# Optimization experiments

Hardware: AMD Instinct MI355X
Metric: run time of the kernel (lower is better)

Reference implementation:

```python
import jax, jax.numpy as jnp
import numpy as np

N_NODES = 100000
N_EDGES = 6400000


def setup_inputs() -> dict:
    key = jax.random.key(0)
    k1, k2, k3, k4, k5, k6 = jax.random.split(key, 6)
    edge_predictions = jax.random.normal(k1, (N_EDGES,), dtype=jnp.float32)
    node_predictions = jax.random.normal(k2, (N_NODES,), dtype=jnp.float32)
    x = jax.random.uniform(k3, (N_NODES, 4), dtype=jnp.float32)  # col 2 = demand
    capacity = jnp.ones((1,), dtype=jnp.float32) * 50.0  # vehicle capacity
    y_edges = (jax.random.uniform(k4, (N_EDGES,)) < 0.1).astype(jnp.float32)
    y_nodes = jax.random.normal(k5, (N_NODES,), dtype=jnp.float32)
    edge_index = jax.random.randint(k6, (2, N_EDGES), 0, N_NODES, dtype=jnp.int64)
    return {
        'edge_predictions': edge_predictions,
        'node_predictions': node_predictions,
        'x': x,
        'capacity': capacity,
        'y_edges': y_edges,
        'y_nodes': y_nodes,
        'edge_index': edge_index,
        'num_nodes': N_NODES,
    }


def _bce_with_logits(logits, targets):
    # numerically stable elementwise BCE-with-logits
    return jnp.maximum(logits, 0.0) - logits * targets + jnp.log1p(jnp.exp(-jnp.abs(logits)))


def _focal_loss(logits, targets, alpha=0.25, gamma=2.0):
    bce = _bce_with_logits(logits, targets)
    probs = jax.nn.sigmoid(logits)
    p_t = probs * targets + (1.0 - probs) * (1.0 - targets)
    alpha_t = alpha * targets + (1.0 - alpha) * (1.0 - targets)
    return jnp.mean(alpha_t * (1.0 - p_t) ** gamma * bce)


def reference(edge_predictions, node_predictions, x, capacity, y_edges, y_nodes,
              edge_index, num_nodes):
    edge_probs = jax.nn.sigmoid(edge_predictions)
    src, dst = edge_index[0], edge_index[1]

    # single segment-sum pass over edges replaces the O(num_nodes * num_edges) loops
    in_sums = jax.ops.segment_sum(edge_probs, dst, num_segments=num_nodes)   # [N]
    out_sums = jax.ops.segment_sum(edge_probs, src, num_segments=num_nodes)  # [N]

    # coverage loss: customer nodes (1..N-1) should have in/out degree-prob == 1
    coverage = (jnp.sum((in_sums[1:] - 1.0) ** 2) + jnp.sum((out_sums[1:] - 1.0) ** 2)) \
               / (2.0 * max(num_nodes - 1, 1))

    # tour formation: flow conservation over ALL nodes
    tour_formation = jnp.sum((in_sums - out_sums) ** 2) / num_nodes

    # depot balance
    depot_balance = (in_sums[0] - out_sums[0]) ** 2

    # capacity tours: depot out-degree ~ ceil(total_demand / capacity)
    demands = x[:, 2]
    total_demand = jnp.sum(demands[1:])
    cap_value = jax.lax.stop_gradient(jnp.mean(capacity))  # torch uses .item()
    expected_tours = jnp.ceil(total_demand / cap_value)
    capacity_tours = (out_sums[0] - expected_tours) ** 2

    # similarity (focal) loss on raw logits
    similarity = _focal_loss(edge_predictions, y_edges, alpha=0.25, gamma=2.0)

    # masked node MSE (mask is data-dependent -> where-based mean)
    mask = (y_nodes >= 0.0).astype(node_predictions.dtype)
    cnt = jnp.maximum(jnp.sum(mask), 1.0)
    node_loss = jnp.sum(mask * (node_predictions - y_nodes) ** 2) / cnt

    total = (coverage * 5.0 + tour_formation * 3.0 + depot_balance * 2.0 +
             capacity_tours * 1.5 + similarity * 0.3 + node_loss * 0.1)
    return total
```

## Files before the change

kernel.cpp:

```cpp
#include <hip/hip_runtime.h>
#include <math.h>

#define RANGE_LOG 9
#define RANGE 512
#define NBUCK_MAX 256
#define CAP 70000u
#define EDGES_PER_CHUNK 4096
#define SCAT_THREADS 512
#define EPT (EDGES_PER_CHUNK / SCAT_THREADS)
#define PELEM (2 * EPT)
#define PARTS 8



__device__ __forceinline__ float wave_reduce_sum(float v) {
    #pragma unroll
    for (int o = 32; o > 0; o >>= 1) v += __shfl_down(v, o, 64);
    return v;
}

template <int NW>
__device__ float block_reduce_sum(float v) {
    __shared__ float s[NW];
    __syncthreads();
    const int lane = threadIdx.x & 63;
    const int wid  = threadIdx.x >> 6;
    v = wave_reduce_sum(v);
    if (lane == 0) s[wid] = v;
    __syncthreads();
    float r = 0.f;
    if (wid == 0) {
        float x = (lane < NW) ? s[lane] : 0.f;
        r = wave_reduce_sum(x);
    }
    return r;
}

__device__ __forceinline__ float focal_term(float x, float t, float p) {
    const float bce = fmaxf(x, 0.f) - x * t + log1pf(expf(-fabsf(x)));
    const float p_t = p * t + (1.f - p) * (1.f - t);
    const float a_t = 0.25f * t + 0.75f * (1.f - t);
    const float om  = 1.f - p_t;
    return a_t * om * om * bce;
}


__global__ __launch_bounds__(SCAT_THREADS, 8)
void scatter_kernel(const float* __restrict__ ep,
                    const float* __restrict__ ye,
                    const int*   __restrict__ ei,
                    unsigned* __restrict__ cursor,
                    unsigned* __restrict__ pairs,
                    float* __restrict__ acc,
                    int E) {
    __shared__ unsigned s_hist[NBUCK_MAX];
    __shared__ unsigned s_cur[NBUCK_MAX];
    __shared__ unsigned s_off[NBUCK_MAX];
    __shared__ unsigned s_gbase[NBUCK_MAX];
    __shared__ unsigned s_pack[2 * EDGES_PER_CHUNK];

    const int tid   = threadIdx.x;
    const int ebase = blockIdx.x * EDGES_PER_CHUNK;
    const int ec    = min(EDGES_PER_CHUNK, E - ebase);
    const int cnt   = 2 * ec;

    if (tid < NBUCK_MAX) s_hist[tid] = 0u;
    __syncthreads();

    unsigned pk[PELEM];
    float local = 0.f;

    #pragma unroll
    for (int k = 0; k < EPT; ++k) {
        const int el = tid + k * SCAT_THREADS;
        if (el < ec) {
            const int e   = ebase + el;
            const float x = ep[e];
            const float t = ye[e];
            const float p = 1.f / (1.f + expf(-x));
            local += focal_term(x, t, p);
            unsigned pq = (unsigned)(p * 16384.f + 0.5f);
            pq = min(pq, 16383u);
            const unsigned s = (unsigned)ei[e];
            const unsigned d = (unsigned)ei[E + e];
            pk[2 * k]     = (s << 15) | pq;
            pk[2 * k + 1] = (d << 15) | 16384u | pq;
            atomicAdd(&s_hist[s >> RANGE_LOG], 1u);
            atomicAdd(&s_hist[d >> RANGE_LOG], 1u);
        }
    }
    __syncthreads();

    if (tid < NBUCK_MAX) s_cur[tid] = s_hist[tid];
    __syncthreads();
    for (int d = 1; d < NBUCK_MAX; d <<= 1) {
        unsigned v = 0u;
        if (tid < NBUCK_MAX) {
            v = s_cur[tid];
            if (tid >= d) v += s_cur[tid - d];
        }
        __syncthreads();
        if (tid < NBUCK_MAX) s_cur[tid] = v;
        __syncthreads();
    }
    if (tid < NBUCK_MAX) {
        const unsigned c    = s_hist[tid];
        const unsigned excl = s_cur[tid] - c;
        s_off[tid]   = excl;
        s_cur[tid]   = excl;
        s_gbase[tid] = c ? atomicAdd(&cursor[tid], c) : 0u;
    }
    __syncthreads();

    #pragma unroll
    for (int k = 0; k < EPT; ++k) {
        const int el = tid + k * SCAT_THREADS;
        if (el < ec) {
            const unsigned a = pk[2 * k];
            const unsigned r0 = atomicAdd(&s_cur[a >> 24], 1u);
            s_pack[r0] = a;
            const unsigned b = pk[2 * k + 1];
            const unsigned r1 = atomicAdd(&s_cur[b >> 24], 1u);
            s_pack[r1] = b;
        }
    }
    __syncthreads();

    for (int idx = tid; idx < cnt; idx += SCAT_THREADS) {
        const unsigned v = s_pack[idx];
        const unsigned b = v >> 24;
        pairs[(size_t)b * CAP + s_gbase[b] + ((unsigned)idx - s_off[b])] = v;
    }

    const float bs = block_reduce_sum<SCAT_THREADS / 64>(local);
    if (tid == 0) atomicAdd(&acc[0], bs);
}

__global__ __launch_bounds__(256)
void accum_kernel(const unsigned* __restrict__ cursor,
                  const unsigned* __restrict__ pairs,
                  float* __restrict__ partials,
                  int N, int nbuck) {
    __shared__ unsigned sAcc[2 * RANGE];
    const int tid  = threadIdx.x;
    const int b    = blockIdx.x % nbuck;
    const int part = blockIdx.x / nbuck;
    for (int i = tid; i < 2 * RANGE; i += 256) sAcc[i] = 0u;
    __syncthreads();

    unsigned fill = cursor[b];
    if (fill > CAP) fill = CAP;
    const unsigned lo = (unsigned)(((unsigned long long)fill * part) / PARTS);
    const unsigned hi = (unsigned)(((unsigned long long)fill * (part + 1)) / PARTS);
    const size_t gb = (size_t)b * CAP;
    for (unsigned i = lo + tid; i < hi; i += 256) {
        const unsigned v     = pairs[gb + i];
        const unsigned local = (v >> 15) & (RANGE - 1);
        const unsigned dir   = (v >> 14) & 1u;
        atomicAdd(&sAcc[dir * RANGE + local], v & 16383u);
    }
    __syncthreads();

    const int nodes = min(RANGE, N - b * RANGE);
    const float inv_scale = 1.f / 16384.f;
    for (int i = tid; i < nodes; i += 256) {
        const int node = b * RANGE + i;
        partials[((size_t)part * 2 + 0) * N + node] = (float)sAcc[i] * inv_scale;
        partials[((size_t)part * 2 + 1) * N + node] = (float)sAcc[RANGE + i] * inv_scale;
    }
}

__global__ void node_cov2_kernel(const float* __restrict__ npred,
                                 const float* __restrict__ yn,
                                 const float* __restrict__ x,
                                 const float* __restrict__ partials,
                                 float* __restrict__ acc,
                                 int N) {
    const int i = blockIdx.x * blockDim.x + threadIdx.x;
    float dem = 0.f, cntm = 0.f, sq = 0.f, cov = 0.f, tour = 0.f;
    if (i < N) {
        float outv = 0.f, inv = 0.f;
        #pragma unroll
        for (int p = 0; p < PARTS; ++p) {
            outv += partials[((size_t)p * 2 + 0) * N + i];
            inv  += partials[((size_t)p * 2 + 1) * N + i];
        }
        if (i >= 1) dem = x[i * 4 + 2];
        const float y = yn[i];
        if (y >= 0.f) {
            cntm = 1.f;
            const float d = npred[i] - y;
            sq = d * d;
        }
        const float dd = inv - outv;
        tour = dd * dd;
        if (i >= 1) cov = (inv - 1.f) * (inv - 1.f) + (outv - 1.f) * (outv - 1.f);
        if (i == 0) { acc[6] = inv; acc[7] = outv; }
    }
    float r;
    r = block_reduce_sum<4>(dem);  if (threadIdx.x == 0) atomicAdd(&acc[1], r);
    r = block_reduce_sum<4>(cntm); if (threadIdx.x == 0) atomicAdd(&acc[2], r);
    r = block_reduce_sum<4>(sq);   if (threadIdx.x == 0) atomicAdd(&acc[3], r);
    r = block_reduce_sum<4>(cov);  if (threadIdx.x == 0) atomicAdd(&acc[4], r);
    r = block_reduce_sum<4>(tour); if (threadIdx.x == 0) atomicAdd(&acc[5], r);
}

__global__ void final2_kernel(const float* __restrict__ acc,
                              const float* __restrict__ capacity,
                              float* __restrict__ out,
                              int N, int E) {
    const float coverage = acc[4] / (2.0f * (float)(N - 1));
    const float tour     = acc[5] / (float)N;
    const float in0  = acc[6];
    const float out0 = acc[7];
    const float depot = (in0 - out0) * (in0 - out0);
    const float cap = capacity[0];
    const float expected = ceilf(acc[1] / cap);
    const float cap_t = (out0 - expected) * (out0 - expected);
    const float sim = acc[0] / (float)E;
    const float node_loss = acc[3] / fmaxf(acc[2], 1.f);
    out[0] = coverage * 5.f + tour * 3.f + depot * 2.f + cap_t * 1.5f +
             sim * 0.3f + node_loss * 0.1f;
}


__global__ void edge_kernel(const float* __restrict__ ep,
                            const float* __restrict__ ye,
                            const int*   __restrict__ src,
                            const int*   __restrict__ dst,
                            float* __restrict__ in_sums,
                            float* __restrict__ out_sums,
                            float* __restrict__ acc,
                            int E) {
    float local = 0.f;
    for (int i = blockIdx.x * blockDim.x + threadIdx.x; i < E;
         i += gridDim.x * blockDim.x) {
        const float x = ep[i];
        const float p = 1.f / (1.f + expf(-x));
        unsafeAtomicAdd(&out_sums[src[i]], p);
        unsafeAtomicAdd(&in_sums[dst[i]], p);
        local += focal_term(x, ye[i], p);
    }
    const float bs = block_reduce_sum<4>(local);
    if (threadIdx.x == 0) atomicAdd(&acc[0], bs);
}

__global__ void node_cov_kernel(const float* __restrict__ npred,
                                const float* __restrict__ yn,
                                const float* __restrict__ x,
                                const float* __restrict__ in_sums,
                                const float* __restrict__ out_sums,
                                float* __restrict__ acc,
                                int N) {
    const int i = blockIdx.x * blockDim.x + threadIdx.x;
    float dem = 0.f, cntm = 0.f, sq = 0.f, cov = 0.f, tour = 0.f;
    if (i < N) {
        if (i >= 1) dem = x[i * 4 + 2];
        const float y = yn[i];
        if (y >= 0.f) {
            cntm = 1.f;
            const float d = npred[i] - y;
            sq = d * d;
        }
        const float a = in_sums[i];
        const float b = out_sums[i];
        const float dd = a - b;
        tour = dd * dd;
        if (i >= 1) cov = (a - 1.f) * (a - 1.f) + (b - 1.f) * (b - 1.f);
        if (i == 0) { acc[6] = a; acc[7] = b; }
    }
    float r;
    r = block_reduce_sum<4>(dem);  if (threadIdx.x == 0) atomicAdd(&acc[1], r);
    r = block_reduce_sum<4>(cntm); if (threadIdx.x == 0) atomicAdd(&acc[2], r);
    r = block_reduce_sum<4>(sq);   if (threadIdx.x == 0) atomicAdd(&acc[3], r);
    r = block_reduce_sum<4>(cov);  if (threadIdx.x == 0) atomicAdd(&acc[4], r);
    r = block_reduce_sum<4>(tour); if (threadIdx.x == 0) atomicAdd(&acc[5], r);
}


extern "C" void kernel_launch(void* const* d_in, const int* in_sizes, int n_in,
                              void* d_out, int out_size, void* d_ws, size_t ws_size,
                              hipStream_t stream) {
    const float* ep       = (const float*)d_in[0];
    const float* npred    = (const float*)d_in[1];
    const float* x        = (const float*)d_in[2];
    const float* capacity = (const float*)d_in[3];
    const float* ye       = (const float*)d_in[4];
    const float* yn       = (const float*)d_in[5];
    const int*   ei       = (const int*)d_in[6];

    const int E = in_sizes[0];
    const int N = in_sizes[1];
    const int nbuck = (N + RANGE - 1) / RANGE;

    char* w = (char*)d_ws;
    float*    acc      = (float*)w;
    unsigned* cursor   = (unsigned*)(w + 256);
    float*    partials = (float*)(w + 4096);
    size_t off_pairs = 4096 + (size_t)PARTS * 2 * N * sizeof(float);
    off_pairs = (off_pairs + 255) & ~(size_t)255;
    unsigned* pairs = (unsigned*)(w + off_pairs);
    const size_t need = off_pairs + (size_t)nbuck * CAP * sizeof(unsigned) + 65536;

    if (nbuck <= NBUCK_MAX && ws_size >= need) {
        hipMemsetAsync(d_ws, 0, 4096, stream);
        const int nchunks = (E + EDGES_PER_CHUNK - 1) / EDGES_PER_CHUNK;
        scatter_kernel<<<nchunks, SCAT_THREADS, 0, stream>>>(
            ep, ye, ei, cursor, pairs, acc, E);
        accum_kernel<<<nbuck * PARTS, 256, 0, stream>>>(
            cursor, pairs, partials, N, nbuck);
        node_cov2_kernel<<<(N + 255) / 256, 256, 0, stream>>>(
            npred, yn, x, partials, acc, N);
        final2_kernel<<<1, 1, 0, stream>>>(acc, capacity, (float*)d_out, N, E);
    } else {
        float* in_sums  = (float*)(w + 4096);
        float* out_sums = in_sums + N;
        hipMemsetAsync(d_ws, 0, 4096 + (size_t)2 * N * sizeof(float), stream);
        edge_kernel<<<4096, 256, 0, stream>>>(ep, ye, ei, ei + E, in_sums,
                                              out_sums, acc, E);
        node_cov_kernel<<<(N + 255) / 256, 256, 0, stream>>>(
            npred, yn, x, in_sums, out_sums, acc, N);
        final2_kernel<<<1, 1, 0, stream>>>(acc, capacity, (float*)d_out, N, E);
    }
}
```

Before: 206.4 us.

## Vectorize edge loads, use fast exp/log intrinsics, interleave integer partials

Each scatter thread now handles eight contiguous edges and reads them with float4/int4 loads instead of strided scalar loads. The sigmoid, softplus and BCE terms now come from hardware exp2, rcp and log intrinsics that share a single exponential. The accumulation kernel reads packed pairs as uint4 and stores interleaved integer out/in partials as uint2, so the node kernel can sum integers and convert to float once. These changes aim to reduce memory instruction count and transcendental cost, at the price of slightly lower-precision math and a new requirement that E be divisible by 4.

```diff
diff --git a/kernel.cpp b/kernel.cpp
--- a/kernel.cpp
+++ b/kernel.cpp
@@ -7,8 +7,7 @@
 #define CAP 70000u
 #define EDGES_PER_CHUNK 4096
 #define SCAT_THREADS 512
-#define EPT (EDGES_PER_CHUNK / SCAT_THREADS)
-#define PELEM (2 * EPT)
+#define EPT 8
 #define PARTS 8
 
 
@@ -36,8 +35,16 @@
     return r;
 }
 
-__device__ __forceinline__ float focal_term(float x, float t, float p) {
-    const float bce = fmaxf(x, 0.f) - x * t + log1pf(expf(-fabsf(x)));
+#define LOG2E 1.44269504f
+#define LN2   0.69314718f
+
+__device__ __forceinline__ float fast_focal(float x, float t, float& p) {
+    const float ax = fabsf(x);
+    const float e  = __builtin_amdgcn_exp2f(-ax * LOG2E);
+    const float r  = __builtin_amdgcn_rcpf(1.f + e);
+    p = (x >= 0.f) ? r : 1.f - r;
+    const float sp  = __builtin_amdgcn_logf(1.f + e) * LN2;
+    const float bce = fmaxf(x, 0.f) - x * t + sp;
     const float p_t = p * t + (1.f - p) * (1.f - t);
     const float a_t = 0.25f * t + 0.75f * (1.f - t);
     const float om  = 1.f - p_t;
@@ -67,26 +74,53 @@
     if (tid < NBUCK_MAX) s_hist[tid] = 0u;
     __syncthreads();
 
-    unsigned pk[PELEM];
+    unsigned pk[2 * EPT];
     float local = 0.f;
-
-    #pragma unroll
-    for (int k = 0; k < EPT; ++k) {
-        const int el = tid + k * SCAT_THREADS;
-        if (el < ec) {
-            const int e   = ebase + el;
-            const float x = ep[e];
-            const float t = ye[e];
-            const float p = 1.f / (1.f + expf(-x));
-            local += focal_term(x, t, p);
-            unsigned pq = (unsigned)(p * 16384.f + 0.5f);
-            pq = min(pq, 16383u);
-            const unsigned s = (unsigned)ei[e];
-            const unsigned d = (unsigned)ei[E + e];
-            pk[2 * k]     = (s << 15) | pq;
-            pk[2 * k + 1] = (d << 15) | 16384u | pq;
-            atomicAdd(&s_hist[s >> RANGE_LOG], 1u);
-            atomicAdd(&s_hist[d >> RANGE_LOG], 1u);
+    const int  le0  = tid * EPT;
+    const bool full = (le0 + EPT) <= ec;
+
+    if (full) {
+        const int e0 = ebase + le0;
+        #pragma unroll
+        for (int h = 0; h < 2; ++h) {
+            const float4 xv = *(const float4*)(ep + e0 + 4 * h);
+            const float4 tv = *(const float4*)(ye + e0 + 4 * h);
+            const int4   sv = *(const int4*)(ei + e0 + 4 * h);
+            const int4   dv = *(const int4*)(ei + E + e0 + 4 * h);
+            const float xx[4] = {xv.x, xv.y, xv.z, xv.w};
+            const float tt[4] = {tv.x, tv.y, tv.z, tv.w};
+            const unsigned ss[4] = {(unsigned)sv.x, (unsigned)sv.y, (unsigned)sv.z, (unsigned)sv.w};
+            const unsigned dd[4] = {(unsigned)dv.x, (unsigned)dv.y, (unsigned)dv.z, (unsigned)dv.w};
+            #pragma unroll
+            for (int j = 0; j < 4; ++j) {
+                float p;
+                local += fast_focal(xx[j], tt[j], p);
+                const unsigned pq = min((unsigned)(p * 16384.f + 0.5f), 16383u);
+                const int k = 4 * h + j;
+                pk[2 * k]     = (ss[j] << 15) | pq;
+                pk[2 * k + 1] = (dd[j] << 15) | 16384u | pq;
+                atomicAdd(&s_hist[ss[j] >> RANGE_LOG], 1u);
+                atomicAdd(&s_hist[dd[j] >> RANGE_LOG], 1u);
+            }
+        }
+    } else {
+        #pragma unroll
+        for (int k = 0; k < EPT; ++k) {
+            pk[2 * k] = 0xFFFFFFFFu;
+            pk[2 * k + 1] = 0xFFFFFFFFu;
+            const int el = le0 + k;
+            if (el < ec) {
+                const int e = ebase + el;
+                float p;
+                local += fast_focal(ep[e], ye[e], p);
+                const unsigned pq = min((unsigned)(p * 16384.f + 0.5f), 16383u);
+                const unsigned s = (unsigned)ei[e];
+                const unsigned d = (unsigned)ei[E + e];
+                pk[2 * k]     = (s << 15) | pq;
+                pk[2 * k + 1] = (d << 15) | 16384u | pq;
+                atomicAdd(&s_hist[s >> RANGE_LOG], 1u);
+                atomicAdd(&s_hist[d >> RANGE_LOG], 1u);
+            }
         }
     }
     __syncthreads();
@@ -112,16 +146,21 @@
     }
     __syncthreads();
 
-    #pragma unroll
-    for (int k = 0; k < EPT; ++k) {
-        const int el = tid + k * SCAT_THREADS;
-        if (el < ec) {
-            const unsigned a = pk[2 * k];
-            const unsigned r0 = atomicAdd(&s_cur[a >> 24], 1u);
-            s_pack[r0] = a;
-            const unsigned b = pk[2 * k + 1];
-            const unsigned r1 = atomicAdd(&s_cur[b >> 24], 1u);
-            s_pack[r1] = b;
+    if (full) {
+        #pragma unroll
+        for (int k = 0; k < 2 * EPT; ++k) {
+            const unsigned v = pk[k];
+            const unsigned r = atomicAdd(&s_cur[v >> 24], 1u);
+            s_pack[r] = v;
+        }
+    } else {
+        #pragma unroll
+        for (int k = 0; k < 2 * EPT; ++k) {
+            const unsigned v = pk[k];
+            if (v != 0xFFFFFFFFu) {
+                const unsigned r = atomicAdd(&s_cur[v >> 24], 1u);
+                s_pack[r] = v;
+            }
         }
     }
     __syncthreads();
@@ -136,10 +175,10 @@
     if (tid == 0) atomicAdd(&acc[0], bs);
 }
 
-__global__ __launch_bounds__(256)
+__global__ __launch_bounds__(256, 8)
 void accum_kernel(const unsigned* __restrict__ cursor,
                   const unsigned* __restrict__ pairs,
-                  float* __restrict__ partials,
+                  unsigned* __restrict__ partials,
                   int N, int nbuck) {
     __shared__ unsigned sAcc[2 * RANGE];
     const int tid  = threadIdx.x;
@@ -150,41 +189,51 @@
 
     unsigned fill = cursor[b];
     if (fill > CAP) fill = CAP;
-    const unsigned lo = (unsigned)(((unsigned long long)fill * part) / PARTS);
-    const unsigned hi = (unsigned)(((unsigned long long)fill * (part + 1)) / PARTS);
+    const unsigned lo = ((unsigned)(((unsigned long long)fill * part) / PARTS)) & ~3u;
+    const unsigned hi = (part == PARTS - 1)
+        ? fill
+        : (((unsigned)(((unsigned long long)fill * (part + 1)) / PARTS)) & ~3u);
     const size_t gb = (size_t)b * CAP;
-    for (unsigned i = lo + tid; i < hi; i += 256) {
-        const unsigned v     = pairs[gb + i];
-        const unsigned local = (v >> 15) & (RANGE - 1);
-        const unsigned dir   = (v >> 14) & 1u;
-        atomicAdd(&sAcc[dir * RANGE + local], v & 16383u);
+    const unsigned hiv = lo + ((hi - lo) & ~3u);
+
+    for (unsigned i = lo + 4 * tid; i < hiv; i += 4 * 256) {
+        const uint4 v = *(const uint4*)(pairs + gb + i);
+        atomicAdd(&sAcc[(v.x >> 14) & 1023u], v.x & 16383u);
+        atomicAdd(&sAcc[(v.y >> 14) & 1023u], v.y & 16383u);
+        atomicAdd(&sAcc[(v.z >> 14) & 1023u], v.z & 16383u);
+        atomicAdd(&sAcc[(v.w >> 14) & 1023u], v.w & 16383u);
+    }
+    for (unsigned i = hiv + tid; i < hi; i += 256) {
+        const unsigned v = pairs[gb + i];
+        atomicAdd(&sAcc[(v >> 14) & 1023u], v & 16383u);
     }
     __syncthreads();
 
     const int nodes = min(RANGE, N - b * RANGE);
-    const float inv_scale = 1.f / 16384.f;
+    unsigned* dstp = partials + (size_t)part * 2 * N + 2 * (size_t)(b * RANGE);
     for (int i = tid; i < nodes; i += 256) {
-        const int node = b * RANGE + i;
-        partials[((size_t)part * 2 + 0) * N + node] = (float)sAcc[i] * inv_scale;
-        partials[((size_t)part * 2 + 1) * N + node] = (float)sAcc[RANGE + i] * inv_scale;
+        *(uint2*)(dstp + 2 * i) = *(const uint2*)(&sAcc[2 * i]);
     }
 }
 
 __global__ void node_cov2_kernel(const float* __restrict__ npred,
                                  const float* __restrict__ yn,
                                  const float* __restrict__ x,
-                                 const float* __restrict__ partials,
+                                 const unsigned* __restrict__ partials,
                                  float* __restrict__ acc,
                                  int N) {
     const int i = blockIdx.x * blockDim.x + threadIdx.x;
     float dem = 0.f, cntm = 0.f, sq = 0.f, cov = 0.f, tour = 0.f;
     if (i < N) {
-        float outv = 0.f, inv = 0.f;
+        unsigned ou = 0u, iu = 0u;
         #pragma unroll
         for (int p = 0; p < PARTS; ++p) {
-            outv += partials[((size_t)p * 2 + 0) * N + i];
-            inv  += partials[((size_t)p * 2 + 1) * N + i];
-        }
+            const uint2 v = *(const uint2*)(partials + (size_t)p * 2 * N + 2 * (size_t)i);
+            ou += v.x;
+            iu += v.y;
+        }
+        const float outv = (float)ou * (1.f / 16384.f);
+        const float inv  = (float)iu * (1.f / 16384.f);
         if (i >= 1) dem = x[i * 4 + 2];
         const float y = yn[i];
         if (y >= 0.f) {
@@ -236,10 +285,10 @@
     for (int i = blockIdx.x * blockDim.x + threadIdx.x; i < E;
          i += gridDim.x * blockDim.x) {
         const float x = ep[i];
-        const float p = 1.f / (1.f + expf(-x));
+        float p;
+        local += fast_focal(x, ye[i], p);
         unsafeAtomicAdd(&out_sums[src[i]], p);
         unsafeAtomicAdd(&in_sums[dst[i]], p);
-        local += focal_term(x, ye[i], p);
     }
     const float bs = block_reduce_sum<4>(local);
     if (threadIdx.x == 0) atomicAdd(&acc[0], bs);
@@ -296,13 +345,13 @@
     char* w = (char*)d_ws;
     float*    acc      = (float*)w;
     unsigned* cursor   = (unsigned*)(w + 256);
-    float*    partials = (float*)(w + 4096);
-    size_t off_pairs = 4096 + (size_t)PARTS * 2 * N * sizeof(float);
+    unsigned* partials = (unsigned*)(w + 4096);
+    size_t off_pairs = 4096 + (size_t)PARTS * 2 * N * sizeof(unsigned);
     off_pairs = (off_pairs + 255) & ~(size_t)255;
     unsigned* pairs = (unsigned*)(w + off_pairs);
     const size_t need = off_pairs + (size_t)nbuck * CAP * sizeof(unsigned) + 65536;
 
-    if (nbuck <= NBUCK_MAX && ws_size >= need) {
+    if (nbuck <= NBUCK_MAX && ws_size >= need && (E % 4) == 0) {
         hipMemsetAsync(d_ws, 0, 4096, stream);
         const int nchunks = (E + EDGES_PER_CHUNK - 1) / EDGES_PER_CHUNK;
         scatter_kernel<<<nchunks, SCAT_THREADS, 0, stream>>>(
```

New measurement: 198.5 us. 1.04x faster.
